# Optimization experiments

Measured on AMD Instinct MI355X. Metric: run time of the kernel, lower is better.

## Reference

```python
import math
import jax, jax.numpy as jnp
import numpy as np

R_MIN, R_MAX, R_BINS = 0.0, 10.0, 64
Z_MIN, Z_MAX, Z_BINS = -2.0, 2.0, 64
DR = (R_MAX - R_MIN) / R_BINS
DZ = (Z_MAX - Z_MIN) / Z_BINS
N = 16777216


def setup_inputs() -> dict:
    key = jax.random.key(0)
    k1, k2 = jax.random.split(key)
    positions = jax.random.normal(k1, (N, 3), dtype=jnp.float32)
    masses = jax.random.uniform(k2, (N,), dtype=jnp.float32)
    return {"positions": positions, "masses": masses}


def _volume():
    redge = R_MIN + jnp.arange(R_BINS + 1, dtype=jnp.float32) * DR
    area = math.pi * (redge[1:] ** 2 - redge[:-1] ** 2)  # [R_BINS]
    return area * DZ


def reference(positions, masses):
    r_cyl = jnp.sqrt(positions[:, 0] ** 2 + positions[:, 1] ** 2)
    i = jnp.floor((r_cyl - R_MIN) / DR).astype(jnp.int32)
    j = jnp.floor((positions[:, 2] - Z_MIN) / DZ).astype(jnp.int32)
    gd = (i >= 0) & (i < R_BINS) & (j >= 0) & (j < Z_BINS)
    flat = jnp.where(gd, i * Z_BINS + j, 0)
    w = jnp.where(gd, masses, 0.0)
    mass_in_bin = jnp.zeros((R_BINS * Z_BINS,), dtype=masses.dtype).at[flat].add(w)
    mass_in_bin = mass_in_bin.reshape(R_BINS, Z_BINS)
    surface_density = mass_in_bin / _volume()[:, None]
    return surface_density
```

## Files before the change

### kernel.cpp

```cpp
#include <hip/hip_runtime.h>
#include <math.h>

#define R_BINS 64
#define Z_BINS 64
#define NBINS (R_BINS * Z_BINS)
#define BLOCK 256
#define GRID 2048
#define NSLAB 64

static constexpr float DR     = 10.0f / 64.0f;
static constexpr float DZ     = 4.0f  / 64.0f;
static constexpr float INV_DR = 6.4f;
static constexpr float INV_DZ = 16.0f;

__device__ __forceinline__ void bin_one(float x, float y, float z, float m,
                                        float* lbins) {
    const float r = sqrtf(x * x + y * y);
    const int i = (int)(r * INV_DR);
    const int j = (int)floorf((z + 2.0f) * INV_DZ);
    if (i < R_BINS && (unsigned)j < (unsigned)Z_BINS) {
        unsafeAtomicAdd(&lbins[i * Z_BINS + j], m);
    }
}

__global__ __launch_bounds__(BLOCK) void hist_kernel(const float4* __restrict__ pos4,
                                                     const float4* __restrict__ mass4,
                                                     float* __restrict__ slabs,
                                                     int n8) {
    __shared__ float lbins[NBINS];
    for (int b = threadIdx.x; b < NBINS; b += BLOCK) lbins[b] = 0.0f;
    __syncthreads();

    const int stride = gridDim.x * BLOCK;
    for (int q = blockIdx.x * BLOCK + threadIdx.x; q < n8; q += stride) {
        const float4* pb = pos4 + (size_t)6 * q;
        const float4 p0 = pb[0];
        const float4 p1 = pb[1];
        const float4 p2 = pb[2];
        const float4 p3 = pb[3];
        const float4 p4 = pb[4];
        const float4 p5 = pb[5];
        const float4 ma = mass4[2 * q];
        const float4 mb = mass4[2 * q + 1];

        bin_one(p0.x, p0.y, p0.z, ma.x, lbins);
        bin_one(p0.w, p1.x, p1.y, ma.y, lbins);
        bin_one(p1.z, p1.w, p2.x, ma.z, lbins);
        bin_one(p2.y, p2.z, p2.w, ma.w, lbins);
        bin_one(p3.x, p3.y, p3.z, mb.x, lbins);
        bin_one(p3.w, p4.x, p4.y, mb.y, lbins);
        bin_one(p4.z, p4.w, p5.x, mb.z, lbins);
        bin_one(p5.y, p5.z, p5.w, mb.w, lbins);
    }

    __syncthreads();
    float* slab = slabs + (size_t)(blockIdx.x % NSLAB) * NBINS;
    for (int b = threadIdx.x; b < NBINS; b += BLOCK) {
        const float v = lbins[b];
        if (v != 0.0f) unsafeAtomicAdd(&slab[b], v);
    }
}

__global__ void tail_kernel(const float* __restrict__ pos,
                            const float* __restrict__ mass,
                            float* __restrict__ slabs,
                            int start, int n) {
    const int t = start + blockIdx.x * blockDim.x + threadIdx.x;
    if (t < n) {
        const float x = pos[3 * t], y = pos[3 * t + 1], z = pos[3 * t + 2];
        const float r = sqrtf(x * x + y * y);
        const int i = (int)(r * INV_DR);
        const int j = (int)floorf((z + 2.0f) * INV_DZ);
        if (i < R_BINS && (unsigned)j < (unsigned)Z_BINS) {
            unsafeAtomicAdd(&slabs[i * Z_BINS + j], mass[t]);
        }
    }
}

__global__ __launch_bounds__(256) void reduce_finalize_kernel(
        const float* __restrict__ slabs, float* __restrict__ out) {
    const int idx = blockIdx.x * blockDim.x + threadIdx.x;
    if (idx < NBINS) {
        float s = 0.0f;
#pragma unroll 8
        for (int k = 0; k < NSLAB; ++k) s += slabs[(size_t)k * NBINS + idx];
        const int i = idx / Z_BINS;
        const float r0 = (float)i * DR;
        const float r1 = (float)(i + 1) * DR;
        const float area = (float)M_PI * (r1 * r1 - r0 * r0);
        out[idx] = s / (area * DZ);
    }
}

extern "C" void kernel_launch(void* const* d_in, const int* in_sizes, int n_in,
                              void* d_out, int out_size, void* d_ws, size_t ws_size,
                              hipStream_t stream) {
    const float* positions = (const float*)d_in[0];
    const float* masses    = (const float*)d_in[1];
    float* out   = (float*)d_out;
    float* slabs = (float*)d_ws;

    const int n = in_sizes[1];
    const int n8 = n / 8;
    const int rem = n - n8 * 8;

    hipMemsetAsync(slabs, 0, (size_t)NSLAB * NBINS * sizeof(float), stream);

    hist_kernel<<<GRID, BLOCK, 0, stream>>>((const float4*)positions,
                                            (const float4*)masses, slabs, n8);
    if (rem > 0) {
        tail_kernel<<<(rem + 255) / 256, 256, 0, stream>>>(positions, masses,
                                                           slabs, n8 * 8, n);
    }
    reduce_finalize_kernel<<<(NBINS + 255) / 256, 256, 0, stream>>>(slabs, out);
}
```

Measured before the change: 328.7 us.

## Replace shared-memory histogram with direct global atomics into 128 slabs

Drops the per-block LDS histogram with its init, flush and barriers, and has every particle atomically add straight into a global slab chosen by block index. The slab count doubles to 128 to spread contention. This trades cheap LDS atomics for global atomics that go through L2. That adds heavy L2 atomic traffic on hot bins (the Gaussian data piles up in the central bins), and the reduce kernel now has to sum twice as many slabs.

Result: slower. 1.211 ms (+268.5%).

```diff
diff --git a/kernel.cpp b/kernel.cpp
--- a/kernel.cpp
+++ b/kernel.cpp
@@ -6,7 +6,7 @@
 #define NBINS (R_BINS * Z_BINS)
 #define BLOCK 256
 #define GRID 2048
-#define NSLAB 64
+#define NSLAB 128
 
 static constexpr float DR     = 10.0f / 64.0f;
 static constexpr float DZ     = 4.0f  / 64.0f;
@@ -14,12 +14,12 @@
 static constexpr float INV_DZ = 16.0f;
 
 __device__ __forceinline__ void bin_one(float x, float y, float z, float m,
-                                        float* lbins) {
+                                        float* __restrict__ slab) {
     const float r = sqrtf(x * x + y * y);
     const int i = (int)(r * INV_DR);
     const int j = (int)floorf((z + 2.0f) * INV_DZ);
     if (i < R_BINS && (unsigned)j < (unsigned)Z_BINS) {
-        unsafeAtomicAdd(&lbins[i * Z_BINS + j], m);
+        unsafeAtomicAdd(&slab[i * Z_BINS + j], m);
     }
 }
 
@@ -27,9 +27,7 @@
                                                      const float4* __restrict__ mass4,
                                                      float* __restrict__ slabs,
                                                      int n8) {
-    __shared__ float lbins[NBINS];
-    for (int b = threadIdx.x; b < NBINS; b += BLOCK) lbins[b] = 0.0f;
-    __syncthreads();
+    float* __restrict__ slab = slabs + (size_t)(blockIdx.x & (NSLAB - 1)) * NBINS;
 
     const int stride = gridDim.x * BLOCK;
     for (int q = blockIdx.x * BLOCK + threadIdx.x; q < n8; q += stride) {
@@ -43,21 +41,14 @@
         const float4 ma = mass4[2 * q];
         const float4 mb = mass4[2 * q + 1];
 
-        bin_one(p0.x, p0.y, p0.z, ma.x, lbins);
-        bin_one(p0.w, p1.x, p1.y, ma.y, lbins);
-        bin_one(p1.z, p1.w, p2.x, ma.z, lbins);
-        bin_one(p2.y, p2.z, p2.w, ma.w, lbins);
-        bin_one(p3.x, p3.y, p3.z, mb.x, lbins);
-        bin_one(p3.w, p4.x, p4.y, mb.y, lbins);
-        bin_one(p4.z, p4.w, p5.x, mb.z, lbins);
-        bin_one(p5.y, p5.z, p5.w, mb.w, lbins);
-    }
-
-    __syncthreads();
-    float* slab = slabs + (size_t)(blockIdx.x % NSLAB) * NBINS;
-    for (int b = threadIdx.x; b < NBINS; b += BLOCK) {
-        const float v = lbins[b];
-        if (v != 0.0f) unsafeAtomicAdd(&slab[b], v);
+        bin_one(p0.x, p0.y, p0.z, ma.x, slab);
+        bin_one(p0.w, p1.x, p1.y, ma.y, slab);
+        bin_one(p1.z, p1.w, p2.x, ma.z, slab);
+        bin_one(p2.y, p2.z, p2.w, ma.w, slab);
+        bin_one(p3.x, p3.y, p3.z, mb.x, slab);
+        bin_one(p3.w, p4.x, p4.y, mb.y, slab);
+        bin_one(p4.z, p4.w, p5.x, mb.z, slab);
+        bin_one(p5.y, p5.z, p5.w, mb.w, slab);
     }
 }
 
```
